# Performance work log

Hardware: AMD Instinct MI355X
Metric: run time of the kernel (lower is better)

Reference implementation:

```python
import jax, jax.numpy as jnp
import numpy as np

N = 100000        # nodes
E = 1_600_000     # edges (avg degree 16)
F_IN = 128        # in_channels
HID = 64          # hidden_channels (per-head)
H1 = 4            # heads layer 1
G = 128           # number of graphs
NEG_SLOPE = 0.2   # PyG GATConv default leaky_relu slope


def setup_inputs() -> dict:
    key = jax.random.key(0)
    ks = jax.random.split(key, 12)
    x = jax.random.normal(ks[0], (N, F_IN), dtype=jnp.float32)
    edge_index = jax.random.randint(ks[1], (2, E), 0, N, dtype=jnp.int64)
    batch = jnp.sort(jax.random.randint(ks[2], (N,), 0, G, dtype=jnp.int64))
    s1 = 1.0 / np.sqrt(F_IN)
    s2 = 1.0 / np.sqrt(H1 * HID)
    # layer 1: in=F_IN, out=H1*HID (PyG lin has no bias; separate bias after concat)
    w1 = jax.random.normal(ks[3], (H1 * HID, F_IN), dtype=jnp.float32) * s1
    a_src1 = jax.random.normal(ks[4], (H1, HID), dtype=jnp.float32) * s1
    a_dst1 = jax.random.normal(ks[5], (H1, HID), dtype=jnp.float32) * s1
    b1 = jnp.zeros((H1 * HID,), dtype=jnp.float32)
    # layer 2: in=H1*HID, out=HID, heads=1
    w2 = jax.random.normal(ks[6], (1 * HID, H1 * HID), dtype=jnp.float32) * s2
    a_src2 = jax.random.normal(ks[7], (1, HID), dtype=jnp.float32) * s2
    a_dst2 = jax.random.normal(ks[8], (1, HID), dtype=jnp.float32) * s2
    b2 = jnp.zeros((HID,), dtype=jnp.float32)
    return {"x": x, "w1": w1, "a_src1": a_src1, "a_dst1": a_dst1, "b1": b1,
            "w2": w2, "a_src2": a_src2, "a_dst2": a_dst2, "b2": b2,
            "edge_index": edge_index, "batch": batch}


def _segment_softmax(alpha, seg, n):
    # numerically-stable softmax of alpha [E,H] grouped by seg (dst node)
    m = jax.ops.segment_max(alpha, seg, num_segments=n)
    m = jnp.where(jnp.isfinite(m), m, 0.0)  # empty segments -> 0
    a = jnp.exp(alpha - m[seg])
    s = jax.ops.segment_sum(a, seg, num_segments=n)
    return a / (s[seg] + 1e-16)


def _gat_conv(x, w, a_src, a_dst, bias, src, dst, n, heads, ch):
    h = (x @ w.T).reshape(n, heads, ch)          # [N,H,C]
    alpha_src = jnp.sum(h * a_src[None], axis=-1)  # [N,H]
    alpha_dst = jnp.sum(h * a_dst[None], axis=-1)  # [N,H]
    e = jax.nn.leaky_relu(alpha_src[src] + alpha_dst[dst], NEG_SLOPE)  # [E,H]
    att = _segment_softmax(e, dst, n)             # [E,H]
    msg = h[src] * att[:, :, None]                # [E,H,C]
    out = jax.ops.segment_sum(msg, dst, num_segments=n)  # [N,H,C]
    return out.reshape(n, heads * ch) + bias


def reference(x, w1, a_src1, a_dst1, b1, w2, a_src2, a_dst2, b2, edge_index, batch):
    src, dst = edge_index[0], edge_index[1]
    h = jax.nn.relu(_gat_conv(x, w1, a_src1, a_dst1, b1, src, dst, N, H1, HID))
    h = jax.nn.relu(_gat_conv(h, w2, a_src2, a_dst2, b2, src, dst, N, 1, HID))
    # global_mean_pool over graph ids
    sums = jax.ops.segment_sum(h, batch, num_segments=G)            # [G,HID]
    cnt = jax.ops.segment_sum(jnp.ones((N,), h.dtype), batch, num_segments=G)
    return sums / jnp.maximum(cnt, 1.0)[:, None]
```

## Files before the change

### kernel.cpp

```cpp
#include <hip/hip_runtime.h>
#include <math.h>
#include <type_traits>

#define NNODES 100000
#define NEDGES 1600000
#define NGRAPH 128
#define NBKT 391
#define CAP 1536
#define EPB 2048

typedef _Float16 f16x4 __attribute__((ext_vector_type(4)));
typedef _Float16 f16x8 __attribute__((ext_vector_type(8)));
typedef float f32x4 __attribute__((ext_vector_type(4)));

__global__ void convert_w(const float* __restrict__ w1, const float* __restrict__ w2,
                          const float* __restrict__ as1c, const float* __restrict__ ad1c,
                          const float* __restrict__ as2c, const float* __restrict__ ad2c,
                          _Float16* __restrict__ w1h, _Float16* __restrict__ w2h,
                          _Float16* __restrict__ va1, _Float16* __restrict__ va2) {
  const int b = blockIdx.x, tid = threadIdx.x;
  if (b < 8) {
    if (tid >= 128) return;
    int h = b & 3;
    const float* coef = (b >= 4) ? ad1c : as1c;
    float s = 0.f;
    for (int c = 0; c < 64; ++c) s = fmaf(w1[(size_t)(h * 64 + c) * 128 + tid], coef[h * 64 + c], s);
    va1[b * 128 + tid] = (_Float16)s;
  } else if (b < 10) {
    int r = b - 8;
    const float* coef = r ? ad2c : as2c;
    float s = 0.f;
    for (int c = 0; c < 64; ++c) s = fmaf(w2[(size_t)c * 256 + tid], coef[c], s);
    va2[r * 256 + tid] = (_Float16)s;
  } else if (b < 138) {
    int i = (b - 10) * 256 + tid;
    w1h[i] = (_Float16)w1[i];
  } else {
    int i = (b - 138) * 256 + tid;
    w2h[i] = (_Float16)w2[i];
  }
}

template <int K, int N, typename AT>
__global__ __launch_bounds__(256) void gemm_mfma(const AT* __restrict__ A,
    const _Float16* __restrict__ Bh, const _Float16* __restrict__ VA,
    _Float16* __restrict__ C, int M, float* __restrict__ asrc, float* __restrict__ adst) {
  constexpr int H = N / 64;
  constexpr int KS = K / 32, NT = N / 16;
  const int lane = threadIdx.x & 63, wid = threadIdx.x >> 6;
  const int lr = lane & 15;
  const int lk = (lane >> 4) * 8;
  const int row = blockIdx.x * 64 + wid * 16 + lr;

  f16x8 a[KS];
  if (row < M) {
    const AT* arow = A + (size_t)row * K;
#pragma unroll
    for (int ks = 0; ks < KS; ++ks) {
      if constexpr (std::is_same<AT, float>::value) {
        float4 v0 = *(const float4*)&arow[ks * 32 + lk];
        float4 v1 = *(const float4*)&arow[ks * 32 + lk + 4];
        f16x8 t;
        t[0] = (_Float16)v0.x; t[1] = (_Float16)v0.y; t[2] = (_Float16)v0.z; t[3] = (_Float16)v0.w;
        t[4] = (_Float16)v1.x; t[5] = (_Float16)v1.y; t[6] = (_Float16)v1.z; t[7] = (_Float16)v1.w;
        a[ks] = t;
      } else {
        a[ks] = *(const f16x8*)&arow[ks * 32 + lk];
      }
    }
  } else {
#pragma unroll
    for (int ks = 0; ks < KS; ++ks) a[ks] = (f16x8){};
  }

  f32x4 accv = (f32x4){0.f, 0.f, 0.f, 0.f};
  {
    const _Float16* vrow = VA + (size_t)lr * K;
#pragma unroll
    for (int ks = 0; ks < KS; ++ks) {
      f16x8 b = *(const f16x8*)&vrow[ks * 32 + lk];
      accv = __builtin_amdgcn_mfma_f32_16x16x32_f16(a[ks], b, accv, 0, 0, 0);
    }
  }

  f32x4 acc[NT];
#pragma unroll
  for (int nt = 0; nt < NT; ++nt) acc[nt] = (f32x4){0.f, 0.f, 0.f, 0.f};
#pragma unroll
  for (int nt = 0; nt < NT; ++nt) {
    const _Float16* brow = Bh + (size_t)(nt * 16 + lr) * K;
#pragma unroll
    for (int ks = 0; ks < KS; ++ks) {
      f16x8 b = *(const f16x8*)&brow[ks * 32 + lk];
      acc[nt] = __builtin_amdgcn_mfma_f32_16x16x32_f16(a[ks], b, acc[nt], 0, 0, 0);
    }
  }

  int row0 = blockIdx.x * 64 + wid * 16 + (lane >> 4) * 4;
#pragma unroll
  for (int r = 0; r < 4; ++r) {
    int orow = row0 + r;
    if (orow >= M) continue;
#pragma unroll
    for (int nt = 0; nt < NT; ++nt)
      C[(size_t)orow * N + nt * 16 + lr] = (_Float16)acc[nt][r];
    if (lr < H) asrc[orow * H + lr] = accv[r];
    else if (lr < 2 * H) adst[orow * H + lr - H] = accv[r];
  }
}

__global__ __launch_bounds__(256) void bucketA(const int* __restrict__ srcv,
    const int* __restrict__ dstv, int2* __restrict__ part, int* __restrict__ gcur,
    int e_count) {
  __shared__ int hist[NBKT];
  __shared__ int base_[NBKT];
  __shared__ int lofs[NBKT];
  const int tid = threadIdx.x;
  const int P = blockIdx.x & 7;
  for (int i = tid; i < NBKT; i += 256) { hist[i] = 0; lofs[i] = 0; }
  __syncthreads();
  const int e0 = blockIdx.x * EPB;
  const int e1 = min(e0 + EPB, e_count);
  for (int e = e0 + tid; e < e1; e += 256) atomicAdd(&hist[dstv[e] >> 8], 1);
  __syncthreads();
  for (int i = tid; i < NBKT; i += 256) {
    int c = hist[i];
    base_[i] = c ? atomicAdd(&gcur[(P * NBKT + i) * 16], c) : 0;
  }
  __syncthreads();
  for (int e = e0 + tid; e < e1; e += 256) {
    int d = dstv[e];
    int b = d >> 8;
    int l = atomicAdd(&lofs[b], 1);
    part[(size_t)(P * NBKT + b) * CAP + base_[b] + l] = make_int2(srcv[e], d);
  }
}

__global__ __launch_bounds__(256) void bucketB1(const int2* __restrict__ part,
    const int* __restrict__ gcur, int* __restrict__ deg, int n) {
  __shared__ int cnt[256];
  const int b = blockIdx.x;
  const int tid = threadIdx.x;
  cnt[tid] = 0;
  __syncthreads();
  for (int P = 0; P < 8; ++P) {
    int cn = gcur[(P * NBKT + b) * 16];
    const int2* seg = part + (size_t)(P * NBKT + b) * CAP;
    for (int i = tid; i < cn; i += 256) atomicAdd(&cnt[seg[i].y & 255], 1);
  }
  __syncthreads();
  int node = (b << 8) + tid;
  if (node < n) deg[node] = cnt[tid];
}

__global__ __launch_bounds__(256) void bucketB2(const int2* __restrict__ part,
    const int* __restrict__ gcur, const int* __restrict__ offsets,
    int* __restrict__ esrc, int n) {
  __shared__ int lcur[256];
  const int b = blockIdx.x;
  const int tid = threadIdx.x;
  int node = (b << 8) + tid;
  lcur[tid] = (node < n) ? offsets[node] : 0;
  __syncthreads();
  for (int P = 0; P < 8; ++P) {
    int cn = gcur[(P * NBKT + b) * 16];
    const int2* seg = part + (size_t)(P * NBKT + b) * CAP;
    for (int i = tid; i < cn; i += 256) {
      int2 e = seg[i];
      int slot = atomicAdd(&lcur[e.y & 255], 1);
      esrc[slot] = e.x;
    }
  }
}

__global__ __launch_bounds__(1024) void scan1(const int* __restrict__ deg, int* __restrict__ inc,
                                              int* __restrict__ bsum, int n) {
  __shared__ int sm[1024];
  int i = blockIdx.x * 1024 + threadIdx.x;
  sm[threadIdx.x] = (i < n) ? deg[i] : 0;
  __syncthreads();
  for (int o = 1; o < 1024; o <<= 1) {
    int t = (threadIdx.x >= o) ? sm[threadIdx.x - o] : 0;
    __syncthreads();
    sm[threadIdx.x] += t;
    __syncthreads();
  }
  if (i < n) inc[i] = sm[threadIdx.x];
  if (threadIdx.x == 1023) bsum[blockIdx.x] = sm[1023];
}

__global__ void scan2(const int* __restrict__ bsum, int* __restrict__ boff, int nb) {
  __shared__ int sm[128];
  int t = threadIdx.x;
  int own = (t < nb) ? bsum[t] : 0;
  sm[t] = own;
  __syncthreads();
  for (int o = 1; o < 128; o <<= 1) {
    int u = (t >= o) ? sm[t - o] : 0;
    __syncthreads();
    sm[t] += u;
    __syncthreads();
  }
  if (t < nb) boff[t] = sm[t] - own;
}

__global__ void scan3(const int* __restrict__ inc, const int* __restrict__ deg,
                      const int* __restrict__ boff, int* __restrict__ offsets,
                      int n, int e_count) {
  int i = blockIdx.x * blockDim.x + threadIdx.x;
  if (i < n) offsets[i] = inc[i] - deg[i] + boff[i >> 10];
  if (i == 0) offsets[n] = e_count;
}

__global__ __launch_bounds__(256) void agg1_kernel(const _Float16* __restrict__ hmat,
    const float* __restrict__ asrc, const float* __restrict__ adst,
    const int* __restrict__ offsets, const int* __restrict__ esrc,
    const float* __restrict__ bias, _Float16* __restrict__ outv) {
  const int lane = threadIdx.x & 63, wid = threadIdx.x >> 6;
  const int node = blockIdx.x * 4 + wid;
  if (node >= NNODES) return;
  const int h = lane >> 4;
  const int start = offsets[node];
  const int end = offsets[node + 1];
  const float adn = adst[node * 4 + h];
  const _Float16* hbase = hmat + lane * 4;
  float acc[4] = {0.f, 0.f, 0.f, 0.f};
  float s = 0.f;
  int j = start;
  for (; j + 8 <= end; j += 8) {
    int sv[8];
#pragma unroll
    for (int t = 0; t < 8; ++t) sv[t] = esrc[j + t];
    f16x4 vv[8];
#pragma unroll
    for (int t = 0; t < 8; ++t) vv[t] = *(const f16x4*)&hbase[(size_t)sv[t] * 256];
    _Float16 ph[8];
#pragma unroll
    for (int t = 0; t < 8; ++t) {
      float v = asrc[sv[t] * 4 + h] + adn;
      v = (v > 0.f) ? v : 0.2f * v;
      float p = __expf(v);
      s += p;
      ph[t] = (_Float16)p;
    }
#pragma unroll
    for (int t = 0; t < 8; ++t)
#pragma unroll
      for (int k = 0; k < 4; ++k)
        acc[k] = fmaf((float)vv[t][k], (float)ph[t], acc[k]);
  }
  for (; j < end; ++j) {
    int sv = esrc[j];
    f16x4 vv = *(const f16x4*)&hbase[(size_t)sv * 256];
    float v = asrc[sv * 4 + h] + adn;
    v = (v > 0.f) ? v : 0.2f * v;
    float p = __expf(v);
    s += p;
    _Float16 phs = (_Float16)p;
#pragma unroll
    for (int k = 0; k < 4; ++k) acc[k] = fmaf((float)vv[k], (float)phs, acc[k]);
  }
  float inv = 1.f / (s + 1e-16f);
  f16x4 ho;
#pragma unroll
  for (int k = 0; k < 4; ++k)
    ho[k] = (_Float16)fmaxf(fmaf(acc[k], inv, bias[lane * 4 + k]), 0.f);
  *(f16x4*)&outv[(size_t)node * 256 + lane * 4] = ho;
}

__global__ __launch_bounds__(256) void agg2_kernel(const _Float16* __restrict__ hmat,
    const float* __restrict__ asrc, const float* __restrict__ adst,
    const int* __restrict__ offsets, const int* __restrict__ esrc,
    const float* __restrict__ bias, float* __restrict__ outv) {
  const int lane = threadIdx.x & 63, wid = threadIdx.x >> 6;
  const int g = lane >> 4, q = lane & 15;
  const int node = blockIdx.x * 16 + wid * 4 + g;
  if (node >= NNODES) return;
  const int start = offsets[node];
  const int end = offsets[node + 1];
  const float adn = adst[node];
  const _Float16* hbase = hmat + q * 4;
  float acc[4] = {0.f, 0.f, 0.f, 0.f};
  float s = 0.f;
  int j = start;
  for (; j + 4 <= end; j += 4) {
    int sv[4];
#pragma unroll
    for (int t = 0; t < 4; ++t) sv[t] = esrc[j + t];
    f16x4 v[4];
#pragma unroll
    for (int t = 0; t < 4; ++t) v[t] = *(const f16x4*)&hbase[(size_t)sv[t] * 64];
#pragma unroll
    for (int t = 0; t < 4; ++t) {
      float x = asrc[sv[t]] + adn;
      x = (x > 0.f) ? x : 0.2f * x;
      float p = __expf(x);
      s += p;
      _Float16 phs = (_Float16)p;
#pragma unroll
      for (int k = 0; k < 4; ++k) acc[k] = fmaf((float)v[t][k], (float)phs, acc[k]);
    }
  }
  for (; j < end; ++j) {
    int sv = esrc[j];
    f16x4 v = *(const f16x4*)&hbase[(size_t)sv * 64];
    float x = asrc[sv] + adn;
    x = (x > 0.f) ? x : 0.2f * x;
    float p = __expf(x);
    s += p;
    _Float16 phs = (_Float16)p;
#pragma unroll
    for (int k = 0; k < 4; ++k) acc[k] = fmaf((float)v[k], (float)phs, acc[k]);
  }
  float inv = 1.f / (s + 1e-16f);
  float4 o;
  o.x = fmaxf(fmaf(acc[0], inv, bias[q * 4 + 0]), 0.f);
  o.y = fmaxf(fmaf(acc[1], inv, bias[q * 4 + 1]), 0.f);
  o.z = fmaxf(fmaf(acc[2], inv, bias[q * 4 + 2]), 0.f);
  o.w = fmaxf(fmaf(acc[3], inv, bias[q * 4 + 3]), 0.f);
  *(float4*)&outv[(size_t)node * 64 + q * 4] = o;
}

__global__ __launch_bounds__(256) void pool_kernel(const float* __restrict__ g2,
    const int* __restrict__ batch, float* __restrict__ out, int n) {
  const int gid = blockIdx.x;
  const int lane = threadIdx.x & 63, w = threadIdx.x >> 6;
  int lo = 0, hi = n;
  while (lo < hi) { int mid = (lo + hi) >> 1; if (batch[mid] < gid) lo = mid + 1; else hi = mid; }
  int lb = lo;
  hi = n;
  while (lo < hi) { int mid = (lo + hi) >> 1; if (batch[mid] < gid + 1) lo = mid + 1; else hi = mid; }
  int ub = lo;
  float acc = 0.f;
  for (int i = lb + w; i < ub; i += 4) acc += g2[(size_t)i * 64 + lane];
  __shared__ float red[4][64];
  red[w][lane] = acc;
  __syncthreads();
  if (threadIdx.x < 64) {
    float sum = (red[0][lane] + red[1][lane]) + (red[2][lane] + red[3][lane]);
    float cnt = fmaxf((float)(ub - lb), 1.f);
    out[gid * 64 + lane] = sum / cnt;
  }
}

extern "C" void kernel_launch(void* const* d_in, const int* in_sizes, int n_in,
                              void* d_out, int out_size, void* d_ws, size_t ws_size,
                              hipStream_t stream) {
  const float* x      = (const float*)d_in[0];
  const float* w1     = (const float*)d_in[1];
  const float* a_src1 = (const float*)d_in[2];
  const float* a_dst1 = (const float*)d_in[3];
  const float* b1     = (const float*)d_in[4];
  const float* w2     = (const float*)d_in[5];
  const float* a_src2 = (const float*)d_in[6];
  const float* a_dst2 = (const float*)d_in[7];
  const float* b2     = (const float*)d_in[8];
  const int*   src    = (const int*)d_in[9];
  const int*   dst    = src + NEDGES;
  const int*   batch  = (const int*)d_in[10];
  float* out = (float*)d_out;

  const int N = NNODES, E = NEDGES;
  const int NB = (N + 1023) / 1024;

  char* wsb = (char*)d_ws;
  size_t off = 0;
  auto alloc = [&](size_t bytes) {
    void* p = wsb + off;
    off = (off + bytes + 255) & ~(size_t)255;
    return p;
  };
  _Float16* h1h = (_Float16*)alloc((size_t)N * 256 * 2);
  _Float16* g1h = (_Float16*)alloc((size_t)N * 256 * 2);
  _Float16* h2h = (_Float16*)alloc((size_t)N * 64 * 2);
  float* g2     = (float*)alloc((size_t)N * 64 * 4);
  float* as1    = (float*)alloc((size_t)N * 4 * 4);
  float* ad1    = (float*)alloc((size_t)N * 4 * 4);
  float* as2    = (float*)alloc((size_t)N * 4);
  float* ad2    = (float*)alloc((size_t)N * 4);
  int* deg      = (int*)alloc((size_t)N * 4);
  int* inc      = (int*)alloc((size_t)N * 4);
  int* bsum     = (int*)alloc((size_t)NB * 4);
  int* boff     = (int*)alloc((size_t)NB * 4);
  int* offsets  = (int*)alloc((size_t)(N + 1) * 4);
  int* esrc     = (int*)alloc((size_t)E * 4);
  int2* part    = (int2*)alloc((size_t)8 * NBKT * CAP * 8);
  int* gcur     = (int*)alloc((size_t)8 * NBKT * 16 * 4);
  _Float16* w1h = (_Float16*)alloc((size_t)256 * 128 * 2);
  _Float16* w2h = (_Float16*)alloc((size_t)64 * 256 * 2);
  _Float16* va1 = (_Float16*)alloc((size_t)16 * 128 * 2);
  _Float16* va2 = (_Float16*)alloc((size_t)16 * 256 * 2);

  hipMemsetAsync(va1, 0, (size_t)16 * 128 * 2, stream);
  hipMemsetAsync(va2, 0, (size_t)16 * 256 * 2, stream);
  convert_w<<<202, 256, 0, stream>>>(w1, w2, a_src1, a_dst1, a_src2, a_dst2,
                                     w1h, w2h, va1, va2);

  hipMemsetAsync(gcur, 0, (size_t)8 * NBKT * 16 * 4, stream);
  bucketA<<<(E + EPB - 1) / EPB, 256, 0, stream>>>(src, dst, part, gcur, E);
  bucketB1<<<NBKT, 256, 0, stream>>>(part, gcur, deg, N);
  scan1<<<NB, 1024, 0, stream>>>(deg, inc, bsum, N);
  scan2<<<1, 128, 0, stream>>>(bsum, boff, NB);
  scan3<<<(N + 255) / 256, 256, 0, stream>>>(inc, deg, boff, offsets, N, E);
  bucketB2<<<NBKT, 256, 0, stream>>>(part, gcur, offsets, esrc, N);

  gemm_mfma<128, 256, float><<<(N + 63) / 64, 256, 0, stream>>>(
      x, w1h, va1, h1h, N, as1, ad1);
  agg1_kernel<<<(N + 3) / 4, 256, 0, stream>>>(h1h, as1, ad1, offsets, esrc, b1, g1h);

  gemm_mfma<256, 64, _Float16><<<(N + 63) / 64, 256, 0, stream>>>(
      g1h, w2h, va2, h2h, N, as2, ad2);
  agg2_kernel<<<(N + 15) / 16, 256, 0, stream>>>(h2h, as2, ad2, offsets, esrc, b2, g2);

  pool_kernel<<<NGRAPH, 256, 0, stream>>>(g2, batch, out, N);
}
```

Measured before the change: 411.2 us.

## Stage GEMM weights in swizzled LDS and make blocks persistent over row groups

The MFMA GEMM kernels now copy the fp16 weight matrix and attention-projection matrix into XOR-swizzled shared memory once per block. Each of 250 blocks then loops over 7 groups of 64 rows, prefetching the next group's A fragment into registers while computing the current one. Output tiles are staged in padded shared memory so they can be written to global memory as coalesced 16-byte chunks. This is meant to remove repeated global/L2 weight fetches and uncoalesced 2-byte stores. In exchange it uses a large LDS footprint (about 80 KB for layer 1), which limits occupancy, and adds extra syncs per group.

```diff
diff --git a/kernel.cpp b/kernel.cpp
--- a/kernel.cpp
+++ b/kernel.cpp
@@ -47,65 +47,105 @@
     _Float16* __restrict__ C, int M, float* __restrict__ asrc, float* __restrict__ adst) {
   constexpr int H = N / 64;
   constexpr int KS = K / 32, NT = N / 16;
-  const int lane = threadIdx.x & 63, wid = threadIdx.x >> 6;
-  const int lr = lane & 15;
-  const int lk = (lane >> 4) * 8;
-  const int row = blockIdx.x * 64 + wid * 16 + lr;
-
-  f16x8 a[KS];
-  if (row < M) {
-    const AT* arow = A + (size_t)row * K;
+  constexpr int BM = 400, NG = 7;
+  constexpr int CP = N + 8;
+  __shared__ _Float16 Bs[N * K];
+  __shared__ _Float16 VAs[16 * K];
+  __shared__ _Float16 Cs[64 * CP];
+  const int tid = threadIdx.x;
+  const int lane = tid & 63, wid = tid >> 6;
+  const int lr = lane & 15, lk = (lane >> 4) * 8;
+  const int bm = blockIdx.x * BM;
+
+  for (int i = tid * 8; i < N * K; i += 2048) {
+    int row = i / K, k = i & (K - 1);
+    f16x8 v = *(const f16x8*)&Bh[i];
+    *(f16x8*)&Bs[(row * K + k) ^ ((row & 7) << 3)] = v;
+  }
+  for (int i = tid * 8; i < 16 * K; i += 2048) {
+    int row = i / K, k = i & (K - 1);
+    f16x8 v = *(const f16x8*)&VA[i];
+    *(f16x8*)&VAs[(row * K + k) ^ ((row & 7) << 3)] = v;
+  }
+  __syncthreads();
+
+  auto loadA = [&](int g, f16x8* areg) {
+    int rlocal = g * 64 + wid * 16 + lr;
+    int row = bm + rlocal;
+    if (rlocal < BM && row < M) {
+      const AT* arow = A + (size_t)row * K;
+#pragma unroll
+      for (int ks = 0; ks < KS; ++ks) {
+        if constexpr (std::is_same<AT, float>::value) {
+          float4 v0 = *(const float4*)&arow[ks * 32 + lk];
+          float4 v1 = *(const float4*)&arow[ks * 32 + lk + 4];
+          f16x8 t;
+          t[0] = (_Float16)v0.x; t[1] = (_Float16)v0.y; t[2] = (_Float16)v0.z; t[3] = (_Float16)v0.w;
+          t[4] = (_Float16)v1.x; t[5] = (_Float16)v1.y; t[6] = (_Float16)v1.z; t[7] = (_Float16)v1.w;
+          areg[ks] = t;
+        } else {
+          areg[ks] = *(const f16x8*)&arow[ks * 32 + lk];
+        }
+      }
+    } else {
+#pragma unroll
+      for (int ks = 0; ks < KS; ++ks) areg[ks] = (f16x8){};
+    }
+  };
+
+  f16x8 a[KS], an[KS];
+  loadA(0, a);
+  const int rl0 = wid * 16 + (lane >> 4) * 4;
+
+  for (int g = 0; g < NG; ++g) {
+    if (g + 1 < NG) loadA(g + 1, an);
+
+    f32x4 accv = (f32x4){0.f, 0.f, 0.f, 0.f};
 #pragma unroll
     for (int ks = 0; ks < KS; ++ks) {
-      if constexpr (std::is_same<AT, float>::value) {
-        float4 v0 = *(const float4*)&arow[ks * 32 + lk];
-        float4 v1 = *(const float4*)&arow[ks * 32 + lk + 4];
-        f16x8 t;
-        t[0] = (_Float16)v0.x; t[1] = (_Float16)v0.y; t[2] = (_Float16)v0.z; t[3] = (_Float16)v0.w;
-        t[4] = (_Float16)v1.x; t[5] = (_Float16)v1.y; t[6] = (_Float16)v1.z; t[7] = (_Float16)v1.w;
-        a[ks] = t;
-      } else {
-        a[ks] = *(const f16x8*)&arow[ks * 32 + lk];
+      f16x8 bv = *(const f16x8*)&VAs[(lr * K + ks * 32 + lk) ^ ((lr & 7) << 3)];
+      accv = __builtin_amdgcn_mfma_f32_16x16x32_f16(a[ks], bv, accv, 0, 0, 0);
+    }
+
+    f32x4 acc[NT];
+#pragma unroll
+    for (int nt = 0; nt < NT; ++nt) acc[nt] = (f32x4){0.f, 0.f, 0.f, 0.f};
+#pragma unroll
+    for (int nt = 0; nt < NT; ++nt) {
+      int brow = nt * 16 + lr;
+#pragma unroll
+      for (int ks = 0; ks < KS; ++ks) {
+        f16x8 b = *(const f16x8*)&Bs[(brow * K + ks * 32 + lk) ^ ((brow & 7) << 3)];
+        acc[nt] = __builtin_amdgcn_mfma_f32_16x16x32_f16(a[ks], b, acc[nt], 0, 0, 0);
       }
     }
-  } else {
-#pragma unroll
-    for (int ks = 0; ks < KS; ++ks) a[ks] = (f16x8){};
-  }
-
-  f32x4 accv = (f32x4){0.f, 0.f, 0.f, 0.f};
-  {
-    const _Float16* vrow = VA + (size_t)lr * K;
-#pragma unroll
-    for (int ks = 0; ks < KS; ++ks) {
-      f16x8 b = *(const f16x8*)&vrow[ks * 32 + lk];
-      accv = __builtin_amdgcn_mfma_f32_16x16x32_f16(a[ks], b, accv, 0, 0, 0);
-    }
-  }
-
-  f32x4 acc[NT];
-#pragma unroll
-  for (int nt = 0; nt < NT; ++nt) acc[nt] = (f32x4){0.f, 0.f, 0.f, 0.f};
-#pragma unroll
-  for (int nt = 0; nt < NT; ++nt) {
-    const _Float16* brow = Bh + (size_t)(nt * 16 + lr) * K;
-#pragma unroll
-    for (int ks = 0; ks < KS; ++ks) {
-      f16x8 b = *(const f16x8*)&brow[ks * 32 + lk];
-      acc[nt] = __builtin_amdgcn_mfma_f32_16x16x32_f16(a[ks], b, acc[nt], 0, 0, 0);
-    }
-  }
-
-  int row0 = blockIdx.x * 64 + wid * 16 + (lane >> 4) * 4;
-#pragma unroll
-  for (int r = 0; r < 4; ++r) {
-    int orow = row0 + r;
-    if (orow >= M) continue;
-#pragma unroll
-    for (int nt = 0; nt < NT; ++nt)
-      C[(size_t)orow * N + nt * 16 + lr] = (_Float16)acc[nt][r];
-    if (lr < H) asrc[orow * H + lr] = accv[r];
-    else if (lr < 2 * H) adst[orow * H + lr - H] = accv[r];
+
+#pragma unroll
+    for (int r = 0; r < 4; ++r) {
+      int rl = rl0 + r;
+#pragma unroll
+      for (int nt = 0; nt < NT; ++nt) Cs[rl * CP + nt * 16 + lr] = (_Float16)acc[nt][r];
+      int rlocal = g * 64 + rl;
+      int row = bm + rlocal;
+      if (rlocal < BM && row < M) {
+        if (lr < H) asrc[row * H + lr] = accv[r];
+        else if (lr < 2 * H) adst[row * H + lr - H] = accv[r];
+      }
+    }
+    __syncthreads();
+
+    int rmax = min(64, min(BM - g * 64, M - (bm + g * 64)));
+    if (rmax > 0) {
+      int nch = rmax * (N / 8);
+      for (int q = tid; q < nch; q += 256) {
+        int row = q / (N / 8), c8 = q % (N / 8);
+        f16x8 v = *(const f16x8*)&Cs[row * CP + c8 * 8];
+        *(f16x8*)&C[(size_t)(bm + g * 64 + row) * N + c8 * 8] = v;
+      }
+    }
+    __syncthreads();
+#pragma unroll
+    for (int ks = 0; ks < KS; ++ks) a[ks] = an[ks];
   }
 }
 
@@ -404,11 +444,11 @@
   scan3<<<(N + 255) / 256, 256, 0, stream>>>(inc, deg, boff, offsets, N, E);
   bucketB2<<<NBKT, 256, 0, stream>>>(part, gcur, offsets, esrc, N);
 
-  gemm_mfma<128, 256, float><<<(N + 63) / 64, 256, 0, stream>>>(
+  gemm_mfma<128, 256, float><<<250, 256, 0, stream>>>(
       x, w1h, va1, h1h, N, as1, ad1);
   agg1_kernel<<<(N + 3) / 4, 256, 0, stream>>>(h1h, as1, ad1, offsets, esrc, b1, g1h);
 
-  gemm_mfma<256, 64, _Float16><<<(N + 63) / 64, 256, 0, stream>>>(
+  gemm_mfma<256, 64, _Float16><<<250, 256, 0, stream>>>(
       g1h, w2h, va2, h2h, N, as2, ad2);
   agg2_kernel<<<(N + 15) / 16, 256, 0, stream>>>(h2h, as2, ad2, offsets, esrc, b2, g2);
 
```

New measurement: 357.2 us. 13.1% less time.
